# Performance work log

Hardware: AMD Instinct MI355X
Metric: run time of the kernel (lower is better)

## Reference

```python
import jax, jax.numpy as jnp
import numpy as np

D_MODEL = 2048
N_Q = 32
N_KV = 8  # num_heads // 4
HEAD_DIM = D_MODEL // N_Q  # 64
CTX = 2048


def precompute_rope_freqs(head_dim, max_seq_len):
    theta = 1.0 / (10000.0 ** (jnp.arange(0, head_dim, 2, dtype=jnp.float32) / head_dim))
    positions = jnp.arange(max_seq_len, dtype=jnp.float32)
    return jnp.outer(positions, theta)  # [T, head_dim//2]


def apply_rope(x, freqs):
    # x: [B, T, H, D]; freqs: [T, D//2]
    T = x.shape[1]
    f = freqs[:T][None, :, None, :]  # [1, T, 1, D//2]
    cos, sin = jnp.cos(f), jnp.sin(f)
    D = x.shape[-1]
    x1, x2 = x[..., : D // 2], x[..., D // 2 :]
    return jnp.concatenate([x1 * cos - x2 * sin, x1 * sin + x2 * cos], axis=-1)


def setup_inputs() -> dict:
    key = jax.random.key(0)
    ks = jax.random.split(key, 10)
    s = 0.02
    B, T = 1, CTX
    inp = {
        "x": jax.random.normal(ks[0], (B, T, D_MODEL), dtype=jnp.float32),
        "Wq": jax.random.normal(ks[1], (D_MODEL, N_Q * HEAD_DIM), dtype=jnp.float32) * s,
        "bq": jnp.zeros((N_Q * HEAD_DIM,), dtype=jnp.float32),
        "Wk": jax.random.normal(ks[2], (D_MODEL, N_KV * HEAD_DIM), dtype=jnp.float32) * s,
        "bk": jnp.zeros((N_KV * HEAD_DIM,), dtype=jnp.float32),
        "Wv": jax.random.normal(ks[3], (D_MODEL, N_KV * HEAD_DIM), dtype=jnp.float32) * s,
        "bv": jnp.zeros((N_KV * HEAD_DIM,), dtype=jnp.float32),
        "Wo": jax.random.normal(ks[4], (D_MODEL, D_MODEL), dtype=jnp.float32) * s,
        "bo": jnp.zeros((D_MODEL,), dtype=jnp.float32),
        "freqs": precompute_rope_freqs(HEAD_DIM, CTX),
    }
    return inp


def reference(x, Wq, bq, Wk, bk, Wv, bv, Wo, bo, freqs):
    B, T, C = x.shape
    q = (x @ Wq + bq).reshape(B, T, N_Q, HEAD_DIM)
    k = (x @ Wk + bk).reshape(B, T, N_KV, HEAD_DIM)
    v = (x @ Wv + bv).reshape(B, T, N_KV, HEAD_DIM)
    q = apply_rope(q, freqs)
    k = apply_rope(k, freqs)
    repeat = N_Q // N_KV
    # repeat_interleave along head dim: q head h uses kv head h // repeat
    k = jnp.repeat(k, repeat, axis=2)
    v = jnp.repeat(v, repeat, axis=2)
    # [B, H, T, D]
    q = q.transpose(0, 2, 1, 3)
    k = k.transpose(0, 2, 1, 3)
    v = v.transpose(0, 2, 1, 3)
    scale = 1.0 / jnp.sqrt(jnp.asarray(HEAD_DIM, dtype=x.dtype))
    scores = jnp.einsum("bhtd,bhsd->bhts", q, k) * scale  # [B, H, T, T]
    causal = jnp.tril(jnp.ones((T, T), dtype=bool))
    scores = jnp.where(causal[None, None], scores, jnp.finfo(scores.dtype).min)
    attn = jax.nn.softmax(scores, axis=-1)
    out = jnp.einsum("bhts,bhsd->bhtd", attn, v)  # [B, H, T, D]
    out = out.transpose(0, 2, 1, 3).reshape(B, T, C)
    return out @ Wo + bo
```

## Files before the change

### kernel.cpp

```cpp
#include <hip/hip_runtime.h>
#include <hip/hip_bf16.h>
#include <math.h>

#define T_CTX 2048
#define DM    2048
#define NQ    32
#define NKV   8
#define HD    64
#define QKV_LD 3072

typedef __attribute__((ext_vector_type(8))) short short8;
typedef __attribute__((ext_vector_type(4))) float floatx4;

__global__ __launch_bounds__(256) void cast_bf16_kernel(const float* __restrict__ src,
                                                        __hip_bfloat16* __restrict__ dst) {
  const int i = blockIdx.x * 256 + threadIdx.x;
  const float4 a = ((const float4*)src)[2 * i];
  const float4 b = ((const float4*)src)[2 * i + 1];
  union { ushort u[8]; short8 v; } o;
  __hip_bfloat16 h;
  h = __float2bfloat16(a.x); o.u[0] = *(ushort*)&h;
  h = __float2bfloat16(a.y); o.u[1] = *(ushort*)&h;
  h = __float2bfloat16(a.z); o.u[2] = *(ushort*)&h;
  h = __float2bfloat16(a.w); o.u[3] = *(ushort*)&h;
  h = __float2bfloat16(b.x); o.u[4] = *(ushort*)&h;
  h = __float2bfloat16(b.y); o.u[5] = *(ushort*)&h;
  h = __float2bfloat16(b.z); o.u[6] = *(ushort*)&h;
  h = __float2bfloat16(b.w); o.u[7] = *(ushort*)&h;
  ((short8*)dst)[i] = o.v;
}

__global__ __launch_bounds__(256) void transpose_cast_kernel(
    const float* __restrict__ src, __hip_bfloat16* __restrict__ dst,
    int Ncols, int Krows) {
  __shared__ float tile[64][65];
  const int n0 = blockIdx.x * 64;
  const int k0 = blockIdx.y * 64;
  const int c = threadIdx.x & 63;
  const int r0 = threadIdx.x >> 6;
#pragma unroll
  for (int s = 0; s < 16; ++s) {
    int r = r0 + 4 * s;
    tile[r][c] = src[(size_t)(k0 + r) * Ncols + n0 + c];
  }
  __syncthreads();
#pragma unroll
  for (int s = 0; s < 16; ++s) {
    int r = r0 + 4 * s;
    dst[(size_t)(n0 + r) * Krows + k0 + c] = __float2bfloat16(tile[c][r]);
  }
}

template <typename OutT>
__global__ __launch_bounds__(256) void gemm_mfma_bt(
    const __hip_bfloat16* __restrict__ A, const __hip_bfloat16* __restrict__ Bt,
    const float* __restrict__ bias, OutT* __restrict__ C, int K, int ldc) {
  __shared__ alignas(16) short As[128 * 64];
  __shared__ alignas(16) short Bs[128 * 64];
  const int tid = threadIdx.x;
  const int lane = tid & 63;
  const int w = tid >> 6;
  const int wr = w >> 1, wc = w & 1;
  const int bm = blockIdx.y * 128, bn = blockIdx.x * 128;

  floatx4 zero4 = {0.f, 0.f, 0.f, 0.f};
  floatx4 acc[4][4];
#pragma unroll
  for (int m = 0; m < 4; ++m)
#pragma unroll
    for (int n = 0; n < 4; ++n) acc[m][n] = zero4;

  const int sr = tid >> 3;
  const int skb = (tid & 7) * 16;
  const int frag_kb = (lane >> 4) * 16;

  for (int k0 = 0; k0 < K; k0 += 64) {
    __syncthreads();
#pragma unroll
    for (int p = 0; p < 4; ++p) {
      const int r = sr + p * 32;
      const short8 av = *(const short8*)((const char*)(A + (size_t)(bm + r) * K + k0) + skb);
      const short8 bv = *(const short8*)((const char*)(Bt + (size_t)(bn + r) * K + k0) + skb);
      const int dst = r * 128 + (skb ^ ((r & 7) << 4));
      *(short8*)((char*)As + dst) = av;
      *(short8*)((char*)Bs + dst) = bv;
    }
    __syncthreads();
#pragma unroll
    for (int h = 0; h < 2; ++h) {
      short8 af[4], bf[4];
      const int kb = h * 64 + frag_kb;
#pragma unroll
      for (int m = 0; m < 4; ++m) {
        const int ar = wr * 64 + m * 16 + (lane & 15);
        af[m] = *(const short8*)((const char*)As + ar * 128 + (kb ^ ((ar & 7) << 4)));
      }
#pragma unroll
      for (int n = 0; n < 4; ++n) {
        const int br = wc * 64 + n * 16 + (lane & 15);
        bf[n] = *(const short8*)((const char*)Bs + br * 128 + (kb ^ ((br & 7) << 4)));
      }
#pragma unroll
      for (int m = 0; m < 4; ++m)
#pragma unroll
        for (int n = 0; n < 4; ++n)
          acc[m][n] = __builtin_amdgcn_mfma_f32_16x16x32_bf16(af[m], bf[n], acc[m][n], 0, 0, 0);
    }
  }

  const int col_l = lane & 15;
  const int row_l = (lane >> 4) * 4;
#pragma unroll
  for (int n = 0; n < 4; ++n) {
    const int col = bn + wc * 64 + n * 16 + col_l;
    const float bv = bias[col];
#pragma unroll
    for (int m = 0; m < 4; ++m) {
      const int row0 = bm + wr * 64 + m * 16 + row_l;
#pragma unroll
      for (int r2 = 0; r2 < 4; ++r2) {
        const float v = acc[m][n][r2] + bv;
        if constexpr (sizeof(OutT) == 2)
          C[(size_t)(row0 + r2) * ldc + col] = __float2bfloat16(v);
        else
          C[(size_t)(row0 + r2) * ldc + col] = v;
      }
    }
  }
}

__global__ __launch_bounds__(256) void rope_kernel(__hip_bfloat16* __restrict__ qkv,
                                                   const float* __restrict__ freqs) {
  const int idx = blockIdx.x * 256 + threadIdx.x;
  const int i = idx & 31;
  const int h = (idx >> 5) % 40;
  const int t = idx / (40 * 32);
  const int base = (h < 32) ? h * HD : DM + (h - 32) * HD;
  __hip_bfloat16* p = qkv + (size_t)t * QKV_LD + base;
  const float f = freqs[t * 32 + i];
  float s, c;
  sincosf(f, &s, &c);
  const float x1 = __bfloat162float(p[i]);
  const float x2 = __bfloat162float(p[i + 32]);
  float r1 = x1 * c - x2 * s;
  float r2 = x1 * s + x2 * c;
  if (h < 32) { r1 *= 0.125f; r2 *= 0.125f; }
  p[i]      = __float2bfloat16(r1);
  p[i + 32] = __float2bfloat16(r2);
}

__global__ __launch_bounds__(256) void attn_mfma_kernel(
    const __hip_bfloat16* __restrict__ qkv, __hip_bfloat16* __restrict__ O) {
  const int bid = blockIdx.x;
  const int head = bid >> 4;
  const int qb = 15 - (bid & 15);
  const int kvh = head >> 2;
  const int tid = threadIdx.x;
  const int lane = tid & 63;
  const int w = tid >> 6;
  const int l15 = lane & 15;
  const int lg = lane >> 4;
  const int qbase = qb * 128 + w * 32;

  __shared__ alignas(16) char Ks[64 * 128];
  __shared__ alignas(16) char Vts[64 * 128];
  __shared__ alignas(16) char Ps[4][32 * 128];

  short8 qf[2][2];
#pragma unroll
  for (int m = 0; m < 2; ++m)
#pragma unroll
    for (int kh = 0; kh < 2; ++kh)
      qf[m][kh] = *(const short8*)(qkv + (size_t)(qbase + m * 16 + l15) * QKV_LD +
                                   head * HD + kh * 32 + lg * 8);

  floatx4 o_acc[2][4];
  float mrow[2][4], lrow[2][4];
#pragma unroll
  for (int m = 0; m < 2; ++m)
#pragma unroll
    for (int n = 0; n < 4; ++n) o_acc[m][n] = floatx4{0.f, 0.f, 0.f, 0.f};
#pragma unroll
  for (int m = 0; m < 2; ++m)
#pragma unroll
    for (int r = 0; r < 4; ++r) { mrow[m][r] = -INFINITY; lrow[m][r] = 0.f; }

  const __hip_bfloat16* Kg = qkv + DM + kvh * HD;
  const __hip_bfloat16* Vg = qkv + DM + NKV * HD + kvh * HD;
  const int nt = 2 * qb + 2;

  for (int kt = 0; kt < nt; ++kt) {
    const int s0 = kt * 64;
    __syncthreads();
#pragma unroll
    for (int p = 0; p < 2; ++p) {
      const int idx = tid + p * 256;
      const int kr = idx >> 3, kc = idx & 7;
      const short8 kv8 = *(const short8*)(Kg + (size_t)(s0 + kr) * QKV_LD + kc * 8);
      *(short8*)(Ks + kr * 128 + ((kc * 16) ^ ((kr & 7) << 4))) = kv8;
    }
    {
      const int vs = tid & 63, d0 = (tid >> 6) * 16;
      const short8 va = *(const short8*)(Vg + (size_t)(s0 + vs) * QKV_LD + d0);
      const short8 vb = *(const short8*)(Vg + (size_t)(s0 + vs) * QKV_LD + d0 + 8);
#pragma unroll
      for (int j = 0; j < 8; ++j) {
        const int rd = d0 + j;
        *(short*)(Vts + rd * 128 + ((vs * 2) ^ ((rd & 7) << 4))) = va[j];
      }
#pragma unroll
      for (int j = 0; j < 8; ++j) {
        const int rd = d0 + 8 + j;
        *(short*)(Vts + rd * 128 + ((vs * 2) ^ ((rd & 7) << 4))) = vb[j];
      }
    }
    __syncthreads();

    if (s0 > qbase + 31) continue;

    floatx4 sacc[2][4];
#pragma unroll
    for (int m = 0; m < 2; ++m)
#pragma unroll
      for (int n = 0; n < 4; ++n) sacc[m][n] = floatx4{0.f, 0.f, 0.f, 0.f};
#pragma unroll
    for (int kh = 0; kh < 2; ++kh) {
      short8 bf[4];
#pragma unroll
      for (int n = 0; n < 4; ++n) {
        const int kr = n * 16 + l15;
        bf[n] = *(const short8*)(Ks + kr * 128 + ((kh * 64 + lg * 16) ^ ((kr & 7) << 4)));
      }
#pragma unroll
      for (int m = 0; m < 2; ++m)
#pragma unroll
        for (int n = 0; n < 4; ++n)
          sacc[m][n] = __builtin_amdgcn_mfma_f32_16x16x32_bf16(qf[m][kh], bf[n], sacc[m][n], 0, 0, 0);
    }
    if (s0 + 63 > qbase) {
#pragma unroll
      for (int m = 0; m < 2; ++m)
#pragma unroll
        for (int n = 0; n < 4; ++n)
#pragma unroll
          for (int r = 0; r < 4; ++r)
            if (s0 + n * 16 + l15 > qbase + m * 16 + lg * 4 + r)
              sacc[m][n][r] = -INFINITY;
    }
#pragma unroll
    for (int m = 0; m < 2; ++m) {
#pragma unroll
      for (int r = 0; r < 4; ++r) {
        float t = fmaxf(fmaxf(sacc[m][0][r], sacc[m][1][r]),
                        fmaxf(sacc[m][2][r], sacc[m][3][r]));
        t = fmaxf(t, __shfl_xor(t, 1));
        t = fmaxf(t, __shfl_xor(t, 2));
        t = fmaxf(t, __shfl_xor(t, 4));
        t = fmaxf(t, __shfl_xor(t, 8));
        const float mn = fmaxf(mrow[m][r], t);
        const float corr = __expf(mrow[m][r] - mn);
        mrow[m][r] = mn;
        float ls = 0.f;
        float pv[4];
#pragma unroll
        for (int n = 0; n < 4; ++n) {
          pv[n] = __expf(sacc[m][n][r] - mn);
          ls += pv[n];
        }
        ls += __shfl_xor(ls, 1);
        ls += __shfl_xor(ls, 2);
        ls += __shfl_xor(ls, 4);
        ls += __shfl_xor(ls, 8);
        lrow[m][r] = lrow[m][r] * corr + ls;
#pragma unroll
        for (int n = 0; n < 4; ++n) o_acc[m][n][r] *= corr;
        const int prow = m * 16 + lg * 4 + r;
#pragma unroll
        for (int n = 0; n < 4; ++n)
          *(__hip_bfloat16*)(Ps[w] + prow * 128 +
                             (((n * 16 + l15) * 2) ^ ((prow & 7) << 4))) =
              __float2bfloat16(pv[n]);
      }
    }
#pragma unroll
    for (int kh = 0; kh < 2; ++kh) {
      short8 pf[2];
#pragma unroll
      for (int m = 0; m < 2; ++m) {
        const int pr = m * 16 + l15;
        pf[m] = *(const short8*)(Ps[w] + pr * 128 + ((kh * 64 + lg * 16) ^ ((pr & 7) << 4)));
      }
      short8 vf[4];
#pragma unroll
      for (int n = 0; n < 4; ++n) {
        const int vr = n * 16 + l15;
        vf[n] = *(const short8*)(Vts + vr * 128 + ((kh * 64 + lg * 16) ^ ((vr & 7) << 4)));
      }
#pragma unroll
      for (int m = 0; m < 2; ++m)
#pragma unroll
        for (int n = 0; n < 4; ++n)
          o_acc[m][n] = __builtin_amdgcn_mfma_f32_16x16x32_bf16(pf[m], vf[n], o_acc[m][n], 0, 0, 0);
    }
  }

#pragma unroll
  for (int m = 0; m < 2; ++m) {
    float inv[4];
#pragma unroll
    for (int r = 0; r < 4; ++r) inv[r] = 1.f / lrow[m][r];
#pragma unroll
    for (int n = 0; n < 4; ++n)
#pragma unroll
      for (int r = 0; r < 4; ++r)
        O[(size_t)(qbase + m * 16 + lg * 4 + r) * DM + head * HD + n * 16 + l15] =
            __float2bfloat16(o_acc[m][n][r] * inv[r]);
  }
}

extern "C" void kernel_launch(void* const* d_in, const int* in_sizes, int n_in,
                              void* d_out, int out_size, void* d_ws, size_t ws_size,
                              hipStream_t stream) {
  const float* x     = (const float*)d_in[0];
  const float* Wq    = (const float*)d_in[1];
  const float* bq    = (const float*)d_in[2];
  const float* Wk    = (const float*)d_in[3];
  const float* bk    = (const float*)d_in[4];
  const float* Wv    = (const float*)d_in[5];
  const float* bv    = (const float*)d_in[6];
  const float* Wo    = (const float*)d_in[7];
  const float* bo    = (const float*)d_in[8];
  const float* freqs = (const float*)d_in[9];
  float* out = (float*)d_out;

  char* ws = (char*)d_ws;
  __hip_bfloat16* qkv  = (__hip_bfloat16*)ws;
  __hip_bfloat16* wt   = (__hip_bfloat16*)(ws + 12582912);
  __hip_bfloat16* xb   = (__hip_bfloat16*)(ws + 25165824);
  __hip_bfloat16* obuf = xb;
  __hip_bfloat16* wot  = wt;
  float*          bcat = (float*)(ws + 33554432);

  const dim3 blk(256);

  cast_bf16_kernel<<<(DM * T_CTX) / (256 * 8), blk, 0, stream>>>(x, xb);
  transpose_cast_kernel<<<dim3(32, 32), blk, 0, stream>>>(Wq, wt, 2048, 2048);
  transpose_cast_kernel<<<dim3(8, 32),  blk, 0, stream>>>(Wk, wt + (size_t)2048 * 2048, 512, 2048);
  transpose_cast_kernel<<<dim3(8, 32),  blk, 0, stream>>>(Wv, wt + (size_t)2560 * 2048, 512, 2048);
  hipMemcpyAsync(bcat,        bq, 2048 * 4, hipMemcpyDeviceToDevice, stream);
  hipMemcpyAsync(bcat + 2048, bk, 512 * 4,  hipMemcpyDeviceToDevice, stream);
  hipMemcpyAsync(bcat + 2560, bv, 512 * 4,  hipMemcpyDeviceToDevice, stream);

  gemm_mfma_bt<__hip_bfloat16><<<dim3(3072 / 128, 2048 / 128), blk, 0, stream>>>(
      xb, wt, bcat, qkv, DM, QKV_LD);

  rope_kernel<<<(T_CTX * 40 * 32) / 256, blk, 0, stream>>>(qkv, freqs);

  transpose_cast_kernel<<<dim3(32, 32), blk, 0, stream>>>(Wo, wot, 2048, 2048);

  attn_mfma_kernel<<<dim3(NQ * 16), blk, 0, stream>>>(qkv, obuf);

  gemm_mfma_bt<float><<<dim3(2048 / 128, 2048 / 128), blk, 0, stream>>>(
      obuf, wot, bo, out, DM, DM);
}
```

Measured before the change: 331.4 us.

## Use direct global-to-LDS loads in GEMM/attention and halve attention query tile

```diff
diff --git a/kernel.cpp b/kernel.cpp
--- a/kernel.cpp
+++ b/kernel.cpp
@@ -11,6 +11,12 @@
 
 typedef __attribute__((ext_vector_type(8))) short short8;
 typedef __attribute__((ext_vector_type(4))) float floatx4;
+
+__device__ __forceinline__ void gload_lds16(const void* g, void* l) {
+  __builtin_amdgcn_global_load_lds(
+      (const __attribute__((address_space(1))) void*)g,
+      (__attribute__((address_space(3))) void*)l, 16, 0, 0);
+}
 
 __global__ __launch_bounds__(256) void cast_bf16_kernel(const float* __restrict__ src,
                                                         __hip_bfloat16* __restrict__ dst) {
@@ -63,27 +69,26 @@
   const int wr = w >> 1, wc = w & 1;
   const int bm = blockIdx.y * 128, bn = blockIdx.x * 128;
 
-  floatx4 zero4 = {0.f, 0.f, 0.f, 0.f};
   floatx4 acc[4][4];
 #pragma unroll
   for (int m = 0; m < 4; ++m)
 #pragma unroll
-    for (int n = 0; n < 4; ++n) acc[m][n] = zero4;
-
-  const int sr = tid >> 3;
-  const int skb = (tid & 7) * 16;
+    for (int n = 0; n < 4; ++n) acc[m][n] = floatx4{0.f, 0.f, 0.f, 0.f};
+
   const int frag_kb = (lane >> 4) * 16;
+  const int srow_in8 = lane >> 3;
+  const int sbyte = (lane & 7) * 16;
 
   for (int k0 = 0; k0 < K; k0 += 64) {
     __syncthreads();
 #pragma unroll
-    for (int p = 0; p < 4; ++p) {
-      const int r = sr + p * 32;
-      const short8 av = *(const short8*)((const char*)(A + (size_t)(bm + r) * K + k0) + skb);
-      const short8 bv = *(const short8*)((const char*)(Bt + (size_t)(bn + r) * K + k0) + skb);
-      const int dst = r * 128 + (skb ^ ((r & 7) << 4));
-      *(short8*)((char*)As + dst) = av;
-      *(short8*)((char*)Bs + dst) = bv;
+    for (int i = 0; i < 4; ++i) {
+      const int r = w * 32 + i * 8 + srow_in8;
+      const int gcb = sbyte ^ ((r & 7) << 4);
+      gload_lds16((const char*)(A + (size_t)(bm + r) * K + k0) + gcb,
+                  (char*)As + (w * 32 + i * 8) * 128);
+      gload_lds16((const char*)(Bt + (size_t)(bn + r) * K + k0) + gcb,
+                  (char*)Bs + (w * 32 + i * 8) * 128);
     }
     __syncthreads();
 #pragma unroll
@@ -152,52 +157,48 @@
 __global__ __launch_bounds__(256) void attn_mfma_kernel(
     const __hip_bfloat16* __restrict__ qkv, __hip_bfloat16* __restrict__ O) {
   const int bid = blockIdx.x;
-  const int head = bid >> 4;
-  const int qb = 15 - (bid & 15);
+  const int head = bid >> 5;
+  const int qb = 31 - (bid & 31);
   const int kvh = head >> 2;
   const int tid = threadIdx.x;
   const int lane = tid & 63;
   const int w = tid >> 6;
   const int l15 = lane & 15;
   const int lg = lane >> 4;
-  const int qbase = qb * 128 + w * 32;
+  const int qbase = qb * 64 + w * 16;
 
   __shared__ alignas(16) char Ks[64 * 128];
   __shared__ alignas(16) char Vts[64 * 128];
-  __shared__ alignas(16) char Ps[4][32 * 128];
-
-  short8 qf[2][2];
-#pragma unroll
-  for (int m = 0; m < 2; ++m)
-#pragma unroll
-    for (int kh = 0; kh < 2; ++kh)
-      qf[m][kh] = *(const short8*)(qkv + (size_t)(qbase + m * 16 + l15) * QKV_LD +
-                                   head * HD + kh * 32 + lg * 8);
-
-  floatx4 o_acc[2][4];
-  float mrow[2][4], lrow[2][4];
-#pragma unroll
-  for (int m = 0; m < 2; ++m)
-#pragma unroll
-    for (int n = 0; n < 4; ++n) o_acc[m][n] = floatx4{0.f, 0.f, 0.f, 0.f};
-#pragma unroll
-  for (int m = 0; m < 2; ++m)
-#pragma unroll
-    for (int r = 0; r < 4; ++r) { mrow[m][r] = -INFINITY; lrow[m][r] = 0.f; }
+  __shared__ alignas(16) char Ps[4][16 * 128];
+
+  short8 qf[2];
+#pragma unroll
+  for (int kh = 0; kh < 2; ++kh)
+    qf[kh] = *(const short8*)(qkv + (size_t)(qbase + l15) * QKV_LD +
+                              head * HD + kh * 32 + lg * 8);
+
+  floatx4 o_acc[4];
+  float mrow[4], lrow[4];
+#pragma unroll
+  for (int n = 0; n < 4; ++n) o_acc[n] = floatx4{0.f, 0.f, 0.f, 0.f};
+#pragma unroll
+  for (int r = 0; r < 4; ++r) { mrow[r] = -INFINITY; lrow[r] = 0.f; }
 
   const __hip_bfloat16* Kg = qkv + DM + kvh * HD;
   const __hip_bfloat16* Vg = qkv + DM + NKV * HD + kvh * HD;
-  const int nt = 2 * qb + 2;
+  const int nt = qb + 1;
+  const int srow_in8 = lane >> 3;
+  const int sbyte = (lane & 7) * 16;
 
   for (int kt = 0; kt < nt; ++kt) {
     const int s0 = kt * 64;
     __syncthreads();
 #pragma unroll
-    for (int p = 0; p < 2; ++p) {
-      const int idx = tid + p * 256;
-      const int kr = idx >> 3, kc = idx & 7;
-      const short8 kv8 = *(const short8*)(Kg + (size_t)(s0 + kr) * QKV_LD + kc * 8);
-      *(short8*)(Ks + kr * 128 + ((kc * 16) ^ ((kr & 7) << 4))) = kv8;
+    for (int i = 0; i < 2; ++i) {
+      const int r = w * 16 + i * 8 + srow_in8;
+      const int gcb = sbyte ^ ((r & 7) << 4);
+      gload_lds16((const char*)(Kg + (size_t)(s0 + r) * QKV_LD) + gcb,
+                  Ks + (w * 16 + i * 8) * 128);
     }
     {
       const int vs = tid & 63, d0 = (tid >> 6) * 16;
@@ -216,13 +217,9 @@
     }
     __syncthreads();
 
-    if (s0 > qbase + 31) continue;
-
-    floatx4 sacc[2][4];
-#pragma unroll
-    for (int m = 0; m < 2; ++m)
-#pragma unroll
-      for (int n = 0; n < 4; ++n) sacc[m][n] = floatx4{0.f, 0.f, 0.f, 0.f};
+    floatx4 sacc[4];
+#pragma unroll
+    for (int n = 0; n < 4; ++n) sacc[n] = floatx4{0.f, 0.f, 0.f, 0.f};
 #pragma unroll
     for (int kh = 0; kh < 2; ++kh) {
       short8 bf[4];
@@ -232,64 +229,53 @@
         bf[n] = *(const short8*)(Ks + kr * 128 + ((kh * 64 + lg * 16) ^ ((kr & 7) << 4)));
       }
 #pragma unroll
-      for (int m = 0; m < 2; ++m)
-#pragma unroll
-        for (int n = 0; n < 4; ++n)
-          sacc[m][n] = __builtin_amdgcn_mfma_f32_16x16x32_bf16(qf[m][kh], bf[n], sacc[m][n], 0, 0, 0);
+      for (int n = 0; n < 4; ++n)
+        sacc[n] = __builtin_amdgcn_mfma_f32_16x16x32_bf16(qf[kh], bf[n], sacc[n], 0, 0, 0);
     }
     if (s0 + 63 > qbase) {
 #pragma unroll
-      for (int m = 0; m < 2; ++m)
-#pragma unroll
-        for (int n = 0; n < 4; ++n)
-#pragma unroll
-          for (int r = 0; r < 4; ++r)
-            if (s0 + n * 16 + l15 > qbase + m * 16 + lg * 4 + r)
-              sacc[m][n][r] = -INFINITY;
-    }
-#pragma unroll
-    for (int m = 0; m < 2; ++m) {
-#pragma unroll
-      for (int r = 0; r < 4; ++r) {
-        float t = fmaxf(fmaxf(sacc[m][0][r], sacc[m][1][r]),
-                        fmaxf(sacc[m][2][r], sacc[m][3][r]));
-        t = fmaxf(t, __shfl_xor(t, 1));
-        t = fmaxf(t, __shfl_xor(t, 2));
-        t = fmaxf(t, __shfl_xor(t, 4));
-        t = fmaxf(t, __shfl_xor(t, 8));
-        const float mn = fmaxf(mrow[m][r], t);
-        const float corr = __expf(mrow[m][r] - mn);
-        mrow[m][r] = mn;
-        float ls = 0.f;
-        float pv[4];
-#pragma unroll
-        for (int n = 0; n < 4; ++n) {
-          pv[n] = __expf(sacc[m][n][r] - mn);
-          ls += pv[n];
-        }
-        ls += __shfl_xor(ls, 1);
-        ls += __shfl_xor(ls, 2);
-        ls += __shfl_xor(ls, 4);
-        ls += __shfl_xor(ls, 8);
-        lrow[m][r] = lrow[m][r] * corr + ls;
-#pragma unroll
-        for (int n = 0; n < 4; ++n) o_acc[m][n][r] *= corr;
-        const int prow = m * 16 + lg * 4 + r;
-#pragma unroll
-        for (int n = 0; n < 4; ++n)
-          *(__hip_bfloat16*)(Ps[w] + prow * 128 +
-                             (((n * 16 + l15) * 2) ^ ((prow & 7) << 4))) =
-              __float2bfloat16(pv[n]);
-      }
+      for (int n = 0; n < 4; ++n)
+#pragma unroll
+        for (int r = 0; r < 4; ++r)
+          if (s0 + n * 16 + l15 > qbase + lg * 4 + r)
+            sacc[n][r] = -INFINITY;
+    }
+#pragma unroll
+    for (int r = 0; r < 4; ++r) {
+      float t = fmaxf(fmaxf(sacc[0][r], sacc[1][r]), fmaxf(sacc[2][r], sacc[3][r]));
+      t = fmaxf(t, __shfl_xor(t, 1));
+      t = fmaxf(t, __shfl_xor(t, 2));
+      t = fmaxf(t, __shfl_xor(t, 4));
+      t = fmaxf(t, __shfl_xor(t, 8));
+      const float mn = fmaxf(mrow[r], t);
+      const float corr = __expf(mrow[r] - mn);
+      mrow[r] = mn;
+      float pv[4];
+      float ls = 0.f;
+#pragma unroll
+      for (int n = 0; n < 4; ++n) {
+        pv[n] = __expf(sacc[n][r] - mn);
+        ls += pv[n];
+      }
+      ls += __shfl_xor(ls, 1);
+      ls += __shfl_xor(ls, 2);
+      ls += __shfl_xor(ls, 4);
+      ls += __shfl_xor(ls, 8);
+      lrow[r] = lrow[r] * corr + ls;
+#pragma unroll
+      for (int n = 0; n < 4; ++n) o_acc[n][r] *= corr;
+      const int prow = lg * 4 + r;
+#pragma unroll
+      for (int n = 0; n < 4; ++n)
+        *(__hip_bfloat16*)(Ps[w] + prow * 128 +
+                           (((n * 16 + l15) * 2) ^ ((prow & 7) << 4))) =
+            __float2bfloat16(pv[n]);
     }
 #pragma unroll
     for (int kh = 0; kh < 2; ++kh) {
-      short8 pf[2];
-#pragma unroll
-      for (int m = 0; m < 2; ++m) {
-        const int pr = m * 16 + l15;
-        pf[m] = *(const short8*)(Ps[w] + pr * 128 + ((kh * 64 + lg * 16) ^ ((pr & 7) << 4)));
-      }
+      const int pr = l15;
+      const short8 pf = *(const short8*)(Ps[w] + pr * 128 +
+                                         ((kh * 64 + lg * 16) ^ ((pr & 7) << 4)));
       short8 vf[4];
 #pragma unroll
       for (int n = 0; n < 4; ++n) {
@@ -297,25 +283,20 @@
         vf[n] = *(const short8*)(Vts + vr * 128 + ((kh * 64 + lg * 16) ^ ((vr & 7) << 4)));
       }
 #pragma unroll
-      for (int m = 0; m < 2; ++m)
-#pragma unroll
-        for (int n = 0; n < 4; ++n)
-          o_acc[m][n] = __builtin_amdgcn_mfma_f32_16x16x32_bf16(pf[m], vf[n], o_acc[m][n], 0, 0, 0);
-    }
-  }
-
-#pragma unroll
-  for (int m = 0; m < 2; ++m) {
-    float inv[4];
-#pragma unroll
-    for (int r = 0; r < 4; ++r) inv[r] = 1.f / lrow[m][r];
-#pragma unroll
-    for (int n = 0; n < 4; ++n)
-#pragma unroll
-      for (int r = 0; r < 4; ++r)
-        O[(size_t)(qbase + m * 16 + lg * 4 + r) * DM + head * HD + n * 16 + l15] =
-            __float2bfloat16(o_acc[m][n][r] * inv[r]);
-  }
+      for (int n = 0; n < 4; ++n)
+        o_acc[n] = __builtin_amdgcn_mfma_f32_16x16x32_bf16(pf, vf[n], o_acc[n], 0, 0, 0);
+    }
+  }
+
+  float inv[4];
+#pragma unroll
+  for (int r = 0; r < 4; ++r) inv[r] = 1.f / lrow[r];
+#pragma unroll
+  for (int n = 0; n < 4; ++n)
+#pragma unroll
+    for (int r = 0; r < 4; ++r)
+      O[(size_t)(qbase + lg * 4 + r) * DM + head * HD + n * 16 + l15] =
+          __float2bfloat16(o_acc[n][r] * inv[r]);
 }
 
 extern "C" void kernel_launch(void* const* d_in, const int* in_sizes, int n_in,
@@ -358,7 +339,7 @@
 
   transpose_cast_kernel<<<dim3(32, 32), blk, 0, stream>>>(Wo, wot, 2048, 2048);
 
-  attn_mfma_kernel<<<dim3(NQ * 16), blk, 0, stream>>>(qkv, obuf);
+  attn_mfma_kernel<<<dim3(NQ * 32), blk, 0, stream>>>(qkv, obuf);
 
   gemm_mfma_bt<float><<<dim3(2048 / 128, 2048 / 128), blk, 0, stream>>>(
       obuf, wot, bo, out, DM, DM);
```

Result: slower. 345.3 us (+4.2%).
